# Kernel tuning notes

Measured on AMD Instinct MI355X. Metric: run time of the kernel, lower is better.

The kernel has to match this reference:

```python
import jax, jax.numpy as jnp
import numpy as np

H = 8  # heads, hard-coded in the original module


def setup_inputs() -> dict:
    key = jax.random.key(0)
    ks = jax.random.split(key, 7)
    B, Lq, Lkv = 4, 2048, 512
    dim_q, dim_kv = 1024, 768
    q = jax.random.normal(ks[0], (B, Lq, dim_q), dtype=jnp.float32)
    kv = jax.random.normal(ks[1], (B, Lkv, dim_kv), dtype=jnp.float32)
    # Linear weights stored as [in, out] so y = x @ W (math-equivalent to torch Linear)
    Wq = jax.random.normal(ks[2], (dim_q, dim_q), dtype=jnp.float32) / np.sqrt(dim_q)
    Wk = jax.random.normal(ks[3], (dim_kv, dim_q), dtype=jnp.float32) / np.sqrt(dim_kv)
    Wv = jax.random.normal(ks[4], (dim_kv, dim_q), dtype=jnp.float32) / np.sqrt(dim_kv)
    Wo = jax.random.normal(ks[5], (dim_q, dim_q), dtype=jnp.float32) / np.sqrt(dim_q)
    bo = jax.random.normal(ks[6], (dim_q,), dtype=jnp.float32) * 0.01
    return {"q": q, "kv": kv, "Wq": Wq, "Wk": Wk, "Wv": Wv, "Wo": Wo, "bo": bo}


def reference(q, kv, Wq, Wk, Wv, Wo, bo):
    B, Lq, dim_q = q.shape
    hd = dim_q // H
    scale = jnp.asarray(hd, q.dtype) ** -0.5
    # projections
    qp = q @ Wq   # [B, Lq, dim_q]
    kp = kv @ Wk  # [B, Lkv, dim_q]
    vp = kv @ Wv  # [B, Lkv, dim_q]
    # split heads: [B, L, H, hd]
    qh = qp.reshape(B, Lq, H, hd)
    kh = kp.reshape(B, kv.shape[1], H, hd)
    vh = vp.reshape(B, kv.shape[1], H, hd)
    # scaled attention scores and softmax
    scores = jnp.einsum("bqhd,bkhd->bhqk", qh, kh) * scale
    attn = jax.nn.softmax(scores, axis=-1)
    out = jnp.einsum("bhqk,bkhd->bqhd", attn, vh).reshape(B, Lq, dim_q)
    return out @ Wo + bo
```

## Files before the change

### kernel.cpp

```cpp
#include <hip/hip_runtime.h>
#include <hip/hip_cooperative_groups.h>

namespace cg = cooperative_groups;


typedef unsigned short u16;
typedef unsigned int u32;
using short8  = __attribute__((ext_vector_type(8))) short;
using floatx4 = __attribute__((ext_vector_type(4))) float;

__device__ inline u16 f2bf(float x) {
  union { float f; u32 u; } v; v.f = x;
  u32 r = (v.u + 0x7fffu + ((v.u >> 16) & 1u)) >> 16;
  return (u16)r;
}

__device__ inline float fast_exp2(float x) {
#if __has_builtin(__builtin_amdgcn_exp2f)
  return __builtin_amdgcn_exp2f(x);
#else
  return exp2f(x);
#endif
}

#define MFMA(a, b, c) __builtin_amdgcn_mfma_f32_16x16x32_bf16(a, b, c, 0, 0, 0)

__device__ inline void async_lds16(const void* g, void* l) {
  __builtin_amdgcn_global_load_lds(
      (const __attribute__((address_space(1))) void*)g,
      (__attribute__((address_space(3))) void*)l, 16, 0, 0);
}

__device__ __forceinline__
void cvt_body(const float* __restrict__ q, const float* __restrict__ kv,
              u16* __restrict__ q_bf, u16* __restrict__ kv_bf, int lin) {
  for (int i = lin * 256 + (int)threadIdx.x; i < 1245184; i += 262144) {
    const float* src; u16* dst; int idx;
    if (i < 1048576) { src = q;  dst = q_bf;  idx = i; }
    else             { src = kv; dst = kv_bf; idx = i - 1048576; }
    float4 a = ((const float4*)src)[2 * idx];
    float4 b = ((const float4*)src)[2 * idx + 1];
    u16 t[8] = {f2bf(a.x), f2bf(a.y), f2bf(a.z), f2bf(a.w),
                f2bf(b.x), f2bf(b.y), f2bf(b.z), f2bf(b.w)};
    ((short8*)dst)[idx] = *(short8*)t;
  }
}

__device__ __forceinline__
void transpose_body(int bid, const float* __restrict__ Wq, const float* __restrict__ Wk,
                    const float* __restrict__ Wv, const float* __restrict__ Wo,
                    u16* __restrict__ WqT, u16* __restrict__ WkvT, u16* __restrict__ WoT,
                    float* __restrict__ tile ) {
  const int z = bid >> 8;
  const float* W; u16* Wt; int K;
  if      (z == 0) { W = Wq; Wt = WqT;               K = 1024; }
  else if (z == 1) { W = Wk; Wt = WkvT;              K = 768;  }
  else if (z == 2) { W = Wv; Wt = WkvT + 1024 * 768; K = 768;  }
  else             { W = Wo; Wt = WoT;               K = 1024; }
  const int k0 = ((bid >> 4) & 15) * 64, n0 = (bid & 15) * 64;
  if (k0 >= K) return;
  const int N = 1024;
  const int t = threadIdx.x;
  for (int p = 0; p < 4; ++p) {
    int cid = p * 256 + t;
    int row = cid >> 4, c = cid & 15;
    float4 v = *(const float4*)&W[(long)(k0 + row) * N + n0 + c * 4];
    tile[row * 68 + c * 4 + 0] = v.x; tile[row * 68 + c * 4 + 1] = v.y;
    tile[row * 68 + c * 4 + 2] = v.z; tile[row * 68 + c * 4 + 3] = v.w;
  }
  __syncthreads();
  for (int p = 0; p < 2; ++p) {
    int oc = p * 256 + t;
    int n = oc >> 3, c = oc & 7;
    u16 tmp[8];
    for (int s = 0; s < 8; ++s) tmp[s] = f2bf(tile[(c * 8 + s) * 68 + n]);
    *(short8*)&Wt[(long)(n0 + n) * K + k0 + c * 8] = *(short8*)tmp;
  }
}

__device__ __forceinline__
void gemm_body(const u16* __restrict__ A, const u16* __restrict__ Bt,
               u16* __restrict__ Cb, float* __restrict__ Cf,
               const float* __restrict__ bias, u16* __restrict__ vt_out,
               int K, int ldc, int lin, int mt_per_xcd, u16* smem) {
  u16* As = smem;
  u16* Bs = smem + 8192;
  const int tid  = threadIdx.x;
  const int wave = tid >> 6, lane = tid & 63;
  const int l15  = lane & 15, quad = lane >> 4;
  const int wm   = (wave >> 1) * 64, wn = (wave & 1) * 64;
  const int xcd  = lin & 7, slot = lin >> 3;
  const int mt   = xcd * mt_per_xcd + (slot % mt_per_xcd);
  const int nti  = slot / mt_per_xcd;
  const long m0  = (long)mt * 128, n0 = (long)nti * 128;
  const int lrow = lane >> 3;
  const int lk   = (((lane & 7) ^ lrow) * 8);
  const int r7   = l15 & 7;

  floatx4 acc[4][4] = {};

  for (int k0 = 0; k0 < K; k0 += 64) {
    for (int c = 0; c < 4; ++c) {
      int rbase = (wave * 4 + c) * 8;
      async_lds16(A  + (m0 + rbase + lrow) * (long)K + k0 + lk, &As[(wave * 4 + c) * 512]);
      async_lds16(Bt + (n0 + rbase + lrow) * (long)K + k0 + lk, &Bs[(wave * 4 + c) * 512]);
    }
    __syncthreads();
    for (int kc = 0; kc < 2; ++kc) {
      short8 af[4], bfr[4];
      for (int i = 0; i < 4; ++i)
        af[i] = *(const short8*)&As[(wm + i * 16 + l15) * 64 + (((kc * 4 + quad) ^ r7) * 8)];
      for (int j = 0; j < 4; ++j)
        bfr[j] = *(const short8*)&Bs[(wn + j * 16 + l15) * 64 + (((kc * 4 + quad) ^ r7) * 8)];
      for (int i = 0; i < 4; ++i)
        for (int j = 0; j < 4; ++j)
          acc[i][j] = MFMA(af[i], bfr[j], acc[i][j]);
    }
    __syncthreads();
  }

  if (Cf) {
    for (int i = 0; i < 4; ++i)
      for (int j = 0; j < 4; ++j) {
        long row = m0 + wm + i * 16 + quad * 4;
        long col = n0 + wn + j * 16 + l15;
        float b = bias ? bias[col] : 0.f;
        for (int r = 0; r < 4; ++r) Cf[(row + r) * (long)ldc + col] = acc[i][j][r] + b;
      }
    return;
  }
  for (int i = 0; i < 4; ++i)
    for (int j = 0; j < 4; ++j)
      for (int r = 0; r < 4; ++r)
        smem[(wm + i * 16 + quad * 4 + r) * 138 + wn + j * 16 + l15] = f2bf(acc[i][j][r]);
  __syncthreads();
  if (vt_out && nti >= 8) {
    const int h  = nti - 8;
    const int bq = (int)(m0 >> 9);
    const int l0 = (int)(m0 & 511);
    u16* vbase = vt_out + ((long)(bq * 8 + h) * 128) * 512;
    for (int p = 0; p < 8; ++p) {
      int cid = p * 256 + tid;
      int d = cid >> 4, c = cid & 15;
      u16 tmp[8];
      for (int s = 0; s < 8; ++s) tmp[s] = smem[(c * 8 + s) * 138 + d];
      *(short8*)&vbase[(long)d * 512 + l0 + c * 8] = *(short8*)tmp;
    }
  } else {
    for (int p = 0; p < 8; ++p) {
      int cid = p * 256 + tid;
      int row = cid >> 4, c = cid & 15;
      short8 v = *(const short8*)&smem[row * 138 + c * 8];
      *(short8*)&Cb[(m0 + row) * (long)ldc + n0 + c * 8] = v;
    }
  }
}

__device__ __forceinline__
void attn_body(const u16* __restrict__ qp, const u16* __restrict__ kp,
               const u16* __restrict__ vT, u16* __restrict__ ctx,
               int lin, u16* smem) {
  u16* Ks = smem;
  u16* Vs = smem + 8192;
  const int tid  = threadIdx.x;
  const int wave = tid >> 6, lane = tid & 63;
  u16* Pw = smem + 16384 + wave * 1024;
  const int l15  = lane & 15, quad = lane >> 4;
  const int xcd  = lin & 7, slot = lin >> 3;
  const int pairIdx = xcd * 4 + (slot & 3);
  const int b = pairIdx >> 3, h = pairIdx & 7;
  const int qtile = slot >> 2;
  const long rowbase = (long)b * 2048 + qtile * 64 + wave * 16;
  const float sc = 0.08838834764831845f * 1.4426950408889634f;

  short8 aQ[4];
  for (int dc = 0; dc < 4; ++dc)
    aQ[dc] = *(const short8*)&qp[(rowbase + l15) * 1024 + h * 128 + dc * 32 + quad * 8];

  floatx4 O[8] = {};
  float lsum[4] = {};
  const u16* kpb   = kp + ((long)b * 512) * 1024 + h * 128;
  const u16* vbase = vT + ((long)(b * 8 + h) * 128) * 512;

  const int krow = lane >> 4;
  const int kpos = lane & 15;
  const int vrow = lane >> 3;
  const int vpos = lane & 7;

  for (int t = 0; t < 8; ++t) {
    for (int i = 0; i < 4; ++i) {
      int inst = wave * 4 + i;
      int row  = inst * 4 + krow;
      int g    = kpos ^ (row & 15);
      async_lds16(kpb + (long)(t * 64 + row) * 1024 + g * 8, &Ks[inst * 512]);
    }
    for (int i = 0; i < 4; ++i) {
      int inst = wave * 4 + i;
      int d    = inst * 8 + vrow;
      int g    = vpos ^ (d & 7);
      async_lds16(vbase + (long)d * 512 + t * 64 + g * 8, &Vs[inst * 512]);
    }
    __syncthreads();

    floatx4 S[4] = {};
    for (int dc = 0; dc < 4; ++dc)
      for (int ks = 0; ks < 4; ++ks) {
        int k = ks * 16 + l15;
        short8 bk = *(const short8*)&Ks[k * 128 + (((dc * 4 + quad) ^ l15) * 8)];
        S[ks] = MFMA(aQ[dc], bk, S[ks]);
      }
    for (int ks = 0; ks < 4; ++ks)
      for (int r = 0; r < 4; ++r) {
        float p = fast_exp2(S[ks][r] * sc);
        lsum[r] += p;
        int row = quad * 4 + r;
        int g   = (ks * 2 + (l15 >> 3)) ^ (row & 7);
        Pw[row * 64 + g * 8 + (l15 & 7)] = f2bf(p);
      }
    short8 aP[2];
    for (int kc = 0; kc < 2; ++kc)
      aP[kc] = *(const short8*)&Pw[l15 * 64 + (((kc * 4 + quad) ^ (l15 & 7)) * 8)];
    for (int j = 0; j < 8; ++j) {
      int d = j * 16 + l15;
      short8 bV0 = *(const short8*)&Vs[d * 64 + ((quad ^ (l15 & 7)) * 8)];
      short8 bV1 = *(const short8*)&Vs[d * 64 + (((4 + quad) ^ (l15 & 7)) * 8)];
      O[j] = MFMA(aP[0], bV0, O[j]);
      O[j] = MFMA(aP[1], bV1, O[j]);
    }
    __syncthreads();
  }

  for (int r = 0; r < 4; ++r) {
    float sum = lsum[r];
    for (int off = 1; off < 16; off <<= 1) sum += __shfl_xor(sum, off);
    lsum[r] = 1.f / sum;
  }
  for (int j = 0; j < 8; ++j)
    for (int r = 0; r < 4; ++r)
      ctx[(rowbase + quad * 4 + r) * 1024 + h * 128 + j * 16 + l15] =
          f2bf(O[j][r] * lsum[r]);
}

__global__ __launch_bounds__(256, 4)
void mega(const float* q, const float* kv, const float* Wq, const float* Wk,
          const float* Wv, const float* Wo,
          u16* q_bf, u16* kv_bf, u16* WqT, u16* WkvT, u16* WoT,
          u16* qp, u16* kp, u16* vT, u16* ctx, float* out, const float* bo) {
  __shared__ __align__(16) u16 smem[20480];
  cg::grid_group g = cg::this_grid();
  const int bid = blockIdx.x;

  cvt_body(q, kv, q_bf, kv_bf, bid);
  transpose_body(bid, Wq, Wk, Wv, Wo, WqT, WkvT, WoT, (float*)smem);
  g.sync();

  if (bid < 768) {
    const bool isQ = bid < 512;
    gemm_body(isQ ? q_bf : kv_bf, isQ ? WqT : WkvT, isQ ? qp : kp,
              nullptr, nullptr, isQ ? (u16*)nullptr : vT,
              isQ ? 1024 : 768, 1024, isQ ? bid : bid - 512, isQ ? 8 : 2, smem);
  }
  g.sync();
  attn_body(qp, kp, vT, ctx, bid, smem);
  g.sync();
  if (bid < 512)
    gemm_body(ctx, WoT, nullptr, out, bo, nullptr, 1024, 1024, bid, 8, smem);
}

__global__ void cvt_all(const float* __restrict__ q, const float* __restrict__ kv,
                        u16* __restrict__ q_bf, u16* __restrict__ kv_bf) {
  int i = blockIdx.x * 256 + threadIdx.x;
  const float* src; u16* dst; int idx;
  if (i < 1048576) { src = q;  dst = q_bf;  idx = i; }
  else             { src = kv; dst = kv_bf; idx = i - 1048576; }
  float4 a = ((const float4*)src)[2 * idx];
  float4 b = ((const float4*)src)[2 * idx + 1];
  u16 t[8] = {f2bf(a.x), f2bf(a.y), f2bf(a.z), f2bf(a.w),
              f2bf(b.x), f2bf(b.y), f2bf(b.z), f2bf(b.w)};
  ((short8*)dst)[idx] = *(short8*)t;
}
__global__ __launch_bounds__(256)
void transpose_all(const float* __restrict__ Wq, const float* __restrict__ Wk,
                   const float* __restrict__ Wv, const float* __restrict__ Wo,
                   u16* __restrict__ WqT, u16* __restrict__ WkvT, u16* __restrict__ WoT) {
  __shared__ __align__(16) float tile[64 * 68];
  int bid = blockIdx.x + blockIdx.y * 16 + blockIdx.z * 256;
  transpose_body(bid, Wq, Wk, Wv, Wo, WqT, WkvT, WoT, tile);
}
__global__ __launch_bounds__(256)
void k_proj_q(const u16* __restrict__ q_bf, const u16* __restrict__ WqT,
              u16* __restrict__ qp) {
  __shared__ __align__(16) u16 smem[17664];
  gemm_body(q_bf, WqT, qp, nullptr, nullptr, nullptr, 1024, 1024, blockIdx.x, 8, smem);
}
__global__ __launch_bounds__(256)
void k_proj_kv(const u16* __restrict__ kv_bf, const u16* __restrict__ WkvT,
               u16* __restrict__ kp, u16* __restrict__ vT) {
  __shared__ __align__(16) u16 smem[17664];
  gemm_body(kv_bf, WkvT, kp, nullptr, nullptr, vT, 768, 1024, blockIdx.x, 2, smem);
}
__global__ __launch_bounds__(256, 4)
void k_attn(const u16* __restrict__ qp, const u16* __restrict__ kp,
            const u16* __restrict__ vT, u16* __restrict__ ctx) {
  __shared__ __align__(16) u16 smem[20480];
  attn_body(qp, kp, vT, ctx, blockIdx.x, smem);
}
__global__ __launch_bounds__(256)
void k_oproj(const u16* __restrict__ ctx, const u16* __restrict__ WoT,
             float* __restrict__ out, const float* __restrict__ bo) {
  __shared__ __align__(16) u16 smem[17664];
  gemm_body(ctx, WoT, nullptr, out, bo, nullptr, 1024, 1024, blockIdx.x, 8, smem);
}

extern "C" void kernel_launch(void* const* d_in, const int* in_sizes, int n_in,
                              void* d_out, int out_size, void* d_ws, size_t ws_size,
                              hipStream_t stream) {
  const float* q  = (const float*)d_in[0];
  const float* kv = (const float*)d_in[1];
  const float* Wq = (const float*)d_in[2];
  const float* Wk = (const float*)d_in[3];
  const float* Wv = (const float*)d_in[4];
  const float* Wo = (const float*)d_in[5];
  const float* bo = (const float*)d_in[6];
  float* out = (float*)d_out;

  char* ws = (char*)d_ws;
  u16* q_bf  = (u16*)(ws + 0);
  u16* kv_bf = (u16*)(ws + 16777216);
  u16* WqT   = (u16*)(ws + 19922944);
  u16* WkvT  = (u16*)(ws + 22020096);
  u16* WoT   = (u16*)(ws + 25165824);
  u16* qp    = (u16*)(ws + 27262976);
  u16* kp    = (u16*)(ws + 44040192);
  u16* vT    = (u16*)(ws + 52428800);
  u16* ctx   = (u16*)(ws + 56623104);

  int maxb = 0;
  hipError_t oe = hipOccupancyMaxActiveBlocksPerMultiprocessor(
      &maxb, (const void*)mega, 256, 0);
  if (oe == hipSuccess && maxb >= 4) {
    void* args[] = {(void*)&q,    (void*)&kv,    (void*)&Wq,   (void*)&Wk,
                    (void*)&Wv,   (void*)&Wo,    (void*)&q_bf, (void*)&kv_bf,
                    (void*)&WqT,  (void*)&WkvT,  (void*)&WoT,  (void*)&qp,
                    (void*)&kp,   (void*)&vT,    (void*)&ctx,  (void*)&out,
                    (void*)&bo};
    hipLaunchCooperativeKernel((const void*)mega, dim3(1024), dim3(256),
                               args, 0, stream);
  } else {
    cvt_all<<<4864, 256, 0, stream>>>(q, kv, q_bf, kv_bf);
    transpose_all<<<dim3(16, 16, 4), 256, 0, stream>>>(Wq, Wk, Wv, Wo, WqT, WkvT, WoT);
    k_proj_q<<<512, 256, 0, stream>>>(q_bf, WqT, qp);
    k_proj_kv<<<256, 256, 0, stream>>>(kv_bf, WkvT, kp, vT);
    k_attn<<<1024, 256, 0, stream>>>(qp, kp, vT, ctx);
    k_oproj<<<512, 256, 0, stream>>>(ctx, WoT, out, bo);
  }
}
```

Before: 200.6 us.

## Split-K the output projection across all blocks, double-buffer GEMM staging, prioritise attention MFMAs

The GEMM inner loop now uses a 32-wide K step with double-buffered LDS staging, so the next tile loads while the current one is computed. In the mega kernel, the output projection previously ran on only 512 of the 1024 blocks. It is now split along K across all 1024 blocks: the upper half writes fp32 partials into reused workspace (qp and q_bf) and raises a flag, and the lower half spins on that flag and adds the partials. The attention loop also raises wave priority around its MFMA sections. The aim is to fill idle CUs during the O-projection and hide load latency, at the cost of flag spin-waits, extra global traffic for the partials, and reliance on all blocks being co-resident.

```diff
diff --git a/kernel.cpp b/kernel.cpp
--- a/kernel.cpp
+++ b/kernel.cpp
@@ -82,9 +82,9 @@
 void gemm_body(const u16* __restrict__ A, const u16* __restrict__ Bt,
                u16* __restrict__ Cb, float* __restrict__ Cf,
                const float* __restrict__ bias, u16* __restrict__ vt_out,
-               int K, int ldc, int lin, int mt_per_xcd, u16* smem) {
-  u16* As = smem;
-  u16* Bs = smem + 8192;
+               int K, int ldc, int lin, int mt_per_xcd, u16* smem,
+               int k_begin, int k_end, float* __restrict__ partial,
+               int* flag, int role) {
   const int tid  = threadIdx.x;
   const int wave = tid >> 6, lane = tid & 63;
   const int l15  = lane & 15, quad = lane >> 4;
@@ -93,30 +93,71 @@
   const int mt   = xcd * mt_per_xcd + (slot % mt_per_xcd);
   const int nti  = slot / mt_per_xcd;
   const long m0  = (long)mt * 128, n0 = (long)nti * 128;
-  const int lrow = lane >> 3;
-  const int lk   = (((lane & 7) ^ lrow) * 8);
-  const int r7   = l15 & 7;
+
+  const int pl  = lane >> 3;
+  const int gg  = (lane & 7) ^ pl;
+  const int ro  = pl * 2 + (gg >> 2);
+  const int co  = (gg & 3) * 8;
+  const u16* Aw = A  + (m0 + wave * 32 + ro) * (long)K + co;
+  const u16* Bw = Bt + (n0 + wave * 32 + ro) * (long)K + co;
+  u16* const A0 = smem;        u16* const B0 = smem + 4096;
+  u16* const A1 = smem + 8192; u16* const B1 = smem + 12288;
+  const int rdo  = ((((l15 & 1) << 2) | quad) ^ (l15 >> 1)) * 8;
+  const int aoff = wm * 32 + (l15 >> 1) * 64 + rdo;
+  const int boff = wn * 32 + (l15 >> 1) * 64 + rdo;
+
+#define STAGE_G(Ab, Bb, kk)                                        \
+  { async_lds16(Aw + (kk),                (Ab) + wave * 1024);       \
+    async_lds16(Aw + 16 * (long)K + (kk), (Ab) + wave * 1024 + 512); \
+    async_lds16(Bw + (kk),                (Bb) + wave * 1024);       \
+    async_lds16(Bw + 16 * (long)K + (kk), (Bb) + wave * 1024 + 512); }
 
   floatx4 acc[4][4] = {};
-
-  for (int k0 = 0; k0 < K; k0 += 64) {
-    for (int c = 0; c < 4; ++c) {
-      int rbase = (wave * 4 + c) * 8;
-      async_lds16(A  + (m0 + rbase + lrow) * (long)K + k0 + lk, &As[(wave * 4 + c) * 512]);
-      async_lds16(Bt + (n0 + rbase + lrow) * (long)K + k0 + lk, &Bs[(wave * 4 + c) * 512]);
-    }
+  STAGE_G(A0, B0, k_begin);
+  const int NS = (k_end - k_begin) >> 5;
+  for (int s = 0; s < NS; ++s) {
     __syncthreads();
-    for (int kc = 0; kc < 2; ++kc) {
-      short8 af[4], bfr[4];
-      for (int i = 0; i < 4; ++i)
-        af[i] = *(const short8*)&As[(wm + i * 16 + l15) * 64 + (((kc * 4 + quad) ^ r7) * 8)];
+    u16* Ac = (s & 1) ? A1 : A0; u16* Bc = (s & 1) ? B1 : B0;
+    if (s + 1 < NS) {
+      u16* An = (s & 1) ? A0 : A1; u16* Bn = (s & 1) ? B0 : B1;
+      STAGE_G(An, Bn, k_begin + (s + 1) * 32);
+    }
+    short8 af[4], bfr[4];
+    for (int i = 0; i < 4; ++i) af[i]  = *(const short8*)&Ac[aoff + i * 512];
+    for (int j = 0; j < 4; ++j) bfr[j] = *(const short8*)&Bc[boff + j * 512];
+    for (int i = 0; i < 4; ++i)
       for (int j = 0; j < 4; ++j)
-        bfr[j] = *(const short8*)&Bs[(wn + j * 16 + l15) * 64 + (((kc * 4 + quad) ^ r7) * 8)];
-      for (int i = 0; i < 4; ++i)
-        for (int j = 0; j < 4; ++j)
-          acc[i][j] = MFMA(af[i], bfr[j], acc[i][j]);
-    }
+        acc[i][j] = MFMA(af[i], bfr[j], acc[i][j]);
+  }
+  __syncthreads();
+#undef STAGE_G
+
+  if (role == 1) {
+    for (int i = 0; i < 4; ++i)
+      for (int j = 0; j < 4; ++j)
+        for (int r = 0; r < 4; ++r)
+          __hip_atomic_store(
+              &partial[(wm + i * 16 + quad * 4 + r) * 128 + wn + j * 16 + l15],
+              acc[i][j][r], __ATOMIC_RELAXED, __HIP_MEMORY_SCOPE_AGENT);
+    __threadfence();
     __syncthreads();
+    if (tid == 0)
+      __hip_atomic_store(flag, 1, __ATOMIC_RELEASE, __HIP_MEMORY_SCOPE_AGENT);
+    return;
+  }
+  if (role == 2) {
+    if (tid == 0)
+      while (__hip_atomic_load(flag, __ATOMIC_ACQUIRE,
+                               __HIP_MEMORY_SCOPE_AGENT) == 0)
+        __builtin_amdgcn_s_sleep(2);
+    __syncthreads();
+    __threadfence();
+    for (int i = 0; i < 4; ++i)
+      for (int j = 0; j < 4; ++j)
+        for (int r = 0; r < 4; ++r)
+          acc[i][j][r] += __hip_atomic_load(
+              &partial[(wm + i * 16 + quad * 4 + r) * 128 + wn + j * 16 + l15],
+              __ATOMIC_RELAXED, __HIP_MEMORY_SCOPE_AGENT);
   }
 
   if (Cf) {
@@ -203,12 +244,14 @@
     __syncthreads();
 
     floatx4 S[4] = {};
+    __builtin_amdgcn_s_setprio(1);
     for (int dc = 0; dc < 4; ++dc)
       for (int ks = 0; ks < 4; ++ks) {
         int k = ks * 16 + l15;
         short8 bk = *(const short8*)&Ks[k * 128 + (((dc * 4 + quad) ^ l15) * 8)];
         S[ks] = MFMA(aQ[dc], bk, S[ks]);
       }
+    __builtin_amdgcn_s_setprio(0);
     for (int ks = 0; ks < 4; ++ks)
       for (int r = 0; r < 4; ++r) {
         float p = fast_exp2(S[ks][r] * sc);
@@ -220,6 +263,7 @@
     short8 aP[2];
     for (int kc = 0; kc < 2; ++kc)
       aP[kc] = *(const short8*)&Pw[l15 * 64 + (((kc * 4 + quad) ^ (l15 & 7)) * 8)];
+    __builtin_amdgcn_s_setprio(1);
     for (int j = 0; j < 8; ++j) {
       int d = j * 16 + l15;
       short8 bV0 = *(const short8*)&Vs[d * 64 + ((quad ^ (l15 & 7)) * 8)];
@@ -227,6 +271,7 @@
       O[j] = MFMA(aP[0], bV0, O[j]);
       O[j] = MFMA(aP[1], bV1, O[j]);
     }
+    __builtin_amdgcn_s_setprio(0);
     __syncthreads();
   }
 
@@ -245,26 +290,38 @@
 void mega(const float* q, const float* kv, const float* Wq, const float* Wk,
           const float* Wv, const float* Wo,
           u16* q_bf, u16* kv_bf, u16* WqT, u16* WkvT, u16* WoT,
-          u16* qp, u16* kp, u16* vT, u16* ctx, float* out, const float* bo) {
+          u16* qp, u16* kp, u16* vT, u16* ctx, float* out, const float* bo,
+          int* flags) {
   __shared__ __align__(16) u16 smem[20480];
   cg::grid_group g = cg::this_grid();
   const int bid = blockIdx.x;
 
   cvt_body(q, kv, q_bf, kv_bf, bid);
   transpose_body(bid, Wq, Wk, Wv, Wo, WqT, WkvT, WoT, (float*)smem);
+  if (bid == 0 && threadIdx.x < 512) flags[threadIdx.x] = 0;
   g.sync();
 
   if (bid < 768) {
     const bool isQ = bid < 512;
     gemm_body(isQ ? q_bf : kv_bf, isQ ? WqT : WkvT, isQ ? qp : kp,
               nullptr, nullptr, isQ ? (u16*)nullptr : vT,
-              isQ ? 1024 : 768, 1024, isQ ? bid : bid - 512, isQ ? 8 : 2, smem);
+              isQ ? 1024 : 768, 1024, isQ ? bid : bid - 512, isQ ? 8 : 2, smem,
+              0, isQ ? 1024 : 768, nullptr, nullptr, 0);
   }
   g.sync();
   attn_body(qp, kp, vT, ctx, bid, smem);
   g.sync();
-  if (bid < 512)
-    gemm_body(ctx, WoT, nullptr, out, bo, nullptr, 1024, 1024, bid, 8, smem);
+  {
+    const int t = (bid < 512) ? bid : bid - 512;
+    float* part = (t < 256) ? ((float*)qp + (long)t * 16384)
+                            : ((float*)q_bf + (long)(t - 256) * 16384);
+    if (bid < 512)
+      gemm_body(ctx, WoT, nullptr, out, bo, nullptr, 1024, 1024, t, 8, smem,
+                0, 512, part, flags + t, 2);
+    else
+      gemm_body(ctx, WoT, nullptr, out, bo, nullptr, 1024, 1024, t, 8, smem,
+                512, 1024, part, flags + t, 1);
+  }
 }
 
 __global__ void cvt_all(const float* __restrict__ q, const float* __restrict__ kv,
@@ -291,13 +348,15 @@
 void k_proj_q(const u16* __restrict__ q_bf, const u16* __restrict__ WqT,
               u16* __restrict__ qp) {
   __shared__ __align__(16) u16 smem[17664];
-  gemm_body(q_bf, WqT, qp, nullptr, nullptr, nullptr, 1024, 1024, blockIdx.x, 8, smem);
+  gemm_body(q_bf, WqT, qp, nullptr, nullptr, nullptr, 1024, 1024, blockIdx.x, 8,
+            smem, 0, 1024, nullptr, nullptr, 0);
 }
 __global__ __launch_bounds__(256)
 void k_proj_kv(const u16* __restrict__ kv_bf, const u16* __restrict__ WkvT,
                u16* __restrict__ kp, u16* __restrict__ vT) {
   __shared__ __align__(16) u16 smem[17664];
-  gemm_body(kv_bf, WkvT, kp, nullptr, nullptr, vT, 768, 1024, blockIdx.x, 2, smem);
+  gemm_body(kv_bf, WkvT, kp, nullptr, nullptr, vT, 768, 1024, blockIdx.x, 2,
+            smem, 0, 768, nullptr, nullptr, 0);
 }
 __global__ __launch_bounds__(256, 4)
 void k_attn(const u16* __restrict__ qp, const u16* __restrict__ kp,
@@ -309,7 +368,8 @@
 void k_oproj(const u16* __restrict__ ctx, const u16* __restrict__ WoT,
              float* __restrict__ out, const float* __restrict__ bo) {
   __shared__ __align__(16) u16 smem[17664];
-  gemm_body(ctx, WoT, nullptr, out, bo, nullptr, 1024, 1024, blockIdx.x, 8, smem);
+  gemm_body(ctx, WoT, nullptr, out, bo, nullptr, 1024, 1024, blockIdx.x, 8,
+            smem, 0, 1024, nullptr, nullptr, 0);
 }
 
 extern "C" void kernel_launch(void* const* d_in, const int* in_sizes, int n_in,
@@ -332,6 +392,7 @@
   u16* WoT   = (u16*)(ws + 25165824);
   u16* qp    = (u16*)(ws + 27262976);
   u16* kp    = (u16*)(ws + 44040192);
+  int* flags = (int*)(ws + 48234496);
   u16* vT    = (u16*)(ws + 52428800);
   u16* ctx   = (u16*)(ws + 56623104);
 
@@ -343,7 +404,7 @@
                     (void*)&Wv,   (void*)&Wo,    (void*)&q_bf, (void*)&kv_bf,
                     (void*)&WqT,  (void*)&WkvT,  (void*)&WoT,  (void*)&qp,
                     (void*)&kp,   (void*)&vT,    (void*)&ctx,  (void*)&out,
-                    (void*)&bo};
+                    (void*)&bo,   (void*)&flags};
     hipLaunchCooperativeKernel((const void*)mega, dim3(1024), dim3(256),
                                args, 0, stream);
   } else {
```

Result: slower. 205.8 us (+2.6%).

## Double-buffer GEMM LDS tiles and overlap K/V loads in attention

Applied to the files above, without the earlier changes.

The GEMM loop now uses two LDS buffers with a 32-wide K step, prefetching the next tile via async global-to-LDS loads while MFMAs run on the current one, synchronised with explicit vmcnt waits and raw barriers. The attention loop staggers K and V staging so the next K block loads during softmax and PV, and the next V block loads during the following QK, with s_setprio raising priority around MFMA sections. The goal is to hide global-load latency that the previous load-then-sync loops exposed. In exchange there are more barriers per iteration, a halved K chunk in the GEMM, and delicate hand-counted waitcnt logic that must match the number of outstanding loads.

```diff
diff --git a/kernel.cpp b/kernel.cpp
--- a/kernel.cpp
+++ b/kernel.cpp
@@ -30,6 +30,13 @@
       (const __attribute__((address_space(1))) void*)g,
       (__attribute__((address_space(3))) void*)l, 16, 0, 0);
 }
+
+#define WAIT_VM(n) { asm volatile("s_waitcnt vmcnt(" #n ")" ::: "memory"); \
+                     __builtin_amdgcn_sched_barrier(0); }
+#define WAIT_LGKM0 { asm volatile("s_waitcnt lgkmcnt(0)" ::: "memory"); \
+                     __builtin_amdgcn_sched_barrier(0); }
+#define SBAR       { __builtin_amdgcn_s_barrier(); \
+                     __builtin_amdgcn_sched_barrier(0); }
 
 __device__ __forceinline__
 void cvt_body(const float* __restrict__ q, const float* __restrict__ kv,
@@ -83,8 +90,6 @@
                u16* __restrict__ Cb, float* __restrict__ Cf,
                const float* __restrict__ bias, u16* __restrict__ vt_out,
                int K, int ldc, int lin, int mt_per_xcd, u16* smem) {
-  u16* As = smem;
-  u16* Bs = smem + 8192;
   const int tid  = threadIdx.x;
   const int wave = tid >> 6, lane = tid & 63;
   const int l15  = lane & 15, quad = lane >> 4;
@@ -93,31 +98,48 @@
   const int mt   = xcd * mt_per_xcd + (slot % mt_per_xcd);
   const int nti  = slot / mt_per_xcd;
   const long m0  = (long)mt * 128, n0 = (long)nti * 128;
-  const int lrow = lane >> 3;
-  const int lk   = (((lane & 7) ^ lrow) * 8);
-  const int r7   = l15 & 7;
+
+  const int pl  = lane >> 3;
+  const int gg  = (lane & 7) ^ pl;
+  const int ro  = pl * 2 + (gg >> 2);
+  const int co  = (gg & 3) * 8;
+  const u16* Aw = A  + (m0 + wave * 32 + ro) * (long)K + co;
+  const u16* Bw = Bt + (n0 + wave * 32 + ro) * (long)K + co;
+  u16* const A0 = smem;        u16* const B0 = smem + 4096;
+  u16* const A1 = smem + 8192; u16* const B1 = smem + 12288;
+  const int rdo  = ((((l15 & 1) << 2) | quad) ^ (l15 >> 1)) * 8;
+  const int aoff = wm * 32 + (l15 >> 1) * 64 + rdo;
+  const int boff = wn * 32 + (l15 >> 1) * 64 + rdo;
+
+#define STAGE_G(Ab, Bb, kk)                                          \
+  { async_lds16(Aw + (kk),                (Ab) + wave * 1024);       \
+    async_lds16(Aw + 16 * (long)K + (kk), (Ab) + wave * 1024 + 512); \
+    async_lds16(Bw + (kk),                (Bb) + wave * 1024);       \
+    async_lds16(Bw + 16 * (long)K + (kk), (Bb) + wave * 1024 + 512); }
 
   floatx4 acc[4][4] = {};
-
-  for (int k0 = 0; k0 < K; k0 += 64) {
-    for (int c = 0; c < 4; ++c) {
-      int rbase = (wave * 4 + c) * 8;
-      async_lds16(A  + (m0 + rbase + lrow) * (long)K + k0 + lk, &As[(wave * 4 + c) * 512]);
-      async_lds16(Bt + (n0 + rbase + lrow) * (long)K + k0 + lk, &Bs[(wave * 4 + c) * 512]);
+  STAGE_G(A0, B0, 0);
+  const int NS = K >> 5;
+  for (int s = 0; s < NS; ++s) {
+    u16* Ac = (s & 1) ? A1 : A0; u16* Bc = (s & 1) ? B1 : B0;
+    if (s + 1 < NS) {
+      u16* An = (s & 1) ? A0 : A1; u16* Bn = (s & 1) ? B0 : B1;
+      STAGE_G(An, Bn, (s + 1) * 32);
+      WAIT_VM(4);
+    } else {
+      WAIT_VM(0);
     }
-    __syncthreads();
-    for (int kc = 0; kc < 2; ++kc) {
-      short8 af[4], bfr[4];
-      for (int i = 0; i < 4; ++i)
-        af[i] = *(const short8*)&As[(wm + i * 16 + l15) * 64 + (((kc * 4 + quad) ^ r7) * 8)];
+    SBAR;
+    short8 af[4], bfr[4];
+    for (int i = 0; i < 4; ++i) af[i]  = *(const short8*)&Ac[aoff + i * 512];
+    for (int j = 0; j < 4; ++j) bfr[j] = *(const short8*)&Bc[boff + j * 512];
+    for (int i = 0; i < 4; ++i)
       for (int j = 0; j < 4; ++j)
-        bfr[j] = *(const short8*)&Bs[(wn + j * 16 + l15) * 64 + (((kc * 4 + quad) ^ r7) * 8)];
-      for (int i = 0; i < 4; ++i)
-        for (int j = 0; j < 4; ++j)
-          acc[i][j] = MFMA(af[i], bfr[j], acc[i][j]);
-    }
-    __syncthreads();
-  }
+        acc[i][j] = MFMA(af[i], bfr[j], acc[i][j]);
+    WAIT_LGKM0;
+    SBAR;
+  }
+#undef STAGE_G
 
   if (Cf) {
     for (int i = 0; i < 4; ++i)
@@ -187,28 +209,38 @@
   const int vrow = lane >> 3;
   const int vpos = lane & 7;
 
+#define STAGE_K(t)                                                             \
+  for (int i = 0; i < 4; ++i) {                                                \
+    int inst = wave * 4 + i;                                                   \
+    int row  = inst * 4 + krow;                                                \
+    int g    = kpos ^ (row & 15);                                              \
+    async_lds16(kpb + (long)((t) * 64 + row) * 1024 + g * 8, &Ks[inst * 512]); \
+  }
+#define STAGE_V(t)                                                             \
+  for (int i = 0; i < 4; ++i) {                                                \
+    int inst = wave * 4 + i;                                                   \
+    int d    = inst * 8 + vrow;                                                \
+    int g    = vpos ^ (d & 7);                                                 \
+    async_lds16(vbase + (long)d * 512 + (t) * 64 + g * 8, &Vs[inst * 512]);    \
+  }
+
+  STAGE_K(0);
+  STAGE_V(0);
   for (int t = 0; t < 8; ++t) {
-    for (int i = 0; i < 4; ++i) {
-      int inst = wave * 4 + i;
-      int row  = inst * 4 + krow;
-      int g    = kpos ^ (row & 15);
-      async_lds16(kpb + (long)(t * 64 + row) * 1024 + g * 8, &Ks[inst * 512]);
-    }
-    for (int i = 0; i < 4; ++i) {
-      int inst = wave * 4 + i;
-      int d    = inst * 8 + vrow;
-      int g    = vpos ^ (d & 7);
-      async_lds16(vbase + (long)d * 512 + t * 64 + g * 8, &Vs[inst * 512]);
-    }
-    __syncthreads();
-
+    WAIT_VM(4);
+    SBAR;
     floatx4 S[4] = {};
+    __builtin_amdgcn_s_setprio(1);
     for (int dc = 0; dc < 4; ++dc)
       for (int ks = 0; ks < 4; ++ks) {
         int k = ks * 16 + l15;
         short8 bk = *(const short8*)&Ks[k * 128 + (((dc * 4 + quad) ^ l15) * 8)];
         S[ks] = MFMA(aQ[dc], bk, S[ks]);
       }
+    __builtin_amdgcn_s_setprio(0);
+    WAIT_LGKM0;
+    SBAR;
+    if (t < 7) STAGE_K(t + 1);
     for (int ks = 0; ks < 4; ++ks)
       for (int r = 0; r < 4; ++r) {
         float p = fast_exp2(S[ks][r] * sc);
@@ -220,6 +252,10 @@
     short8 aP[2];
     for (int kc = 0; kc < 2; ++kc)
       aP[kc] = *(const short8*)&Pw[l15 * 64 + (((kc * 4 + quad) ^ (l15 & 7)) * 8)];
+    if (t < 7) { WAIT_VM(4); }
+    else       { WAIT_VM(0); }
+    SBAR;
+    __builtin_amdgcn_s_setprio(1);
     for (int j = 0; j < 8; ++j) {
       int d = j * 16 + l15;
       short8 bV0 = *(const short8*)&Vs[d * 64 + ((quad ^ (l15 & 7)) * 8)];
@@ -227,8 +263,13 @@
       O[j] = MFMA(aP[0], bV0, O[j]);
       O[j] = MFMA(aP[1], bV1, O[j]);
     }
-    __syncthreads();
-  }
+    __builtin_amdgcn_s_setprio(0);
+    WAIT_LGKM0;
+    SBAR;
+    if (t < 7) STAGE_V(t + 1);
+  }
+#undef STAGE_K
+#undef STAGE_V
 
   for (int r = 0; r < 4; ++r) {
     float sum = lsum[r];
```

After: 199.1 us. About the same (-0.7%).
